# Kernel tuning notes

Measured on AMD Instinct MI355X. Metric: run time of the kernel, lower is better.

Reference implementation:

```python
import jax, jax.numpy as jnp
import numpy as np

B, S, E, H = 4, 2048, 1024, 16
DH = E // H  # 64
DF = 4 * E   # 4096
EPS = 1e-5


def layer_norm(x, g, b):
    mu = jnp.mean(x, axis=-1, keepdims=True)
    var = jnp.mean(jnp.square(x - mu), axis=-1, keepdims=True)
    return (x - mu) * jax.lax.rsqrt(var + EPS) * g + b


def setup_inputs() -> dict:
    key = jax.random.key(0)
    ks = jax.random.split(key, 16)
    s_e = 1.0 / np.sqrt(E)
    s_f = 1.0 / np.sqrt(DF)
    inp = {
        "x": jax.random.normal(ks[0], (B, S, E), jnp.float32),
        # per-head projections stacked over heads: [H, E, DH]
        "wq": jax.random.normal(ks[1], (H, E, DH), jnp.float32) * s_e,
        "wk": jax.random.normal(ks[2], (H, E, DH), jnp.float32) * s_e,
        "wv": jax.random.normal(ks[3], (H, E, DH), jnp.float32) * s_e,
        # output projection [H*DH, E] with bias
        "wo": jax.random.normal(ks[4], (H * DH, E), jnp.float32) * s_e,
        "bo": jax.random.normal(ks[5], (E,), jnp.float32) * 0.01,
        # SwiGLU FFN
        "w1": jax.random.normal(ks[6], (E, DF), jnp.float32) * s_e,
        "b1": jax.random.normal(ks[7], (DF,), jnp.float32) * 0.01,
        "w2": jax.random.normal(ks[8], (E, DF), jnp.float32) * s_e,
        "b2": jax.random.normal(ks[9], (DF,), jnp.float32) * 0.01,
        "w3": jax.random.normal(ks[10], (DF, E), jnp.float32) * s_f,
        "b3": jax.random.normal(ks[11], (E,), jnp.float32) * 0.01,
        # LayerNorm params
        "g1": jnp.ones((E,), jnp.float32),
        "be1": jnp.zeros((E,), jnp.float32),
        "g2": jnp.ones((E,), jnp.float32),
        "be2": jnp.zeros((E,), jnp.float32),
    }
    return inp


def reference(x, wq, wk, wv, wo, bo, w1, b1, w2, b2, w3, b3, g1, be1, g2, be2):
    # --- LN1 + multi-head causal attention ---
    h = layer_norm(x, g1, be1)                       # [B,S,E]
    q = jnp.einsum('bse,hed->bhsd', h, wq)           # [B,H,S,DH]
    k = jnp.einsum('bse,hed->bhsd', h, wk)
    v = jnp.einsum('bse,hed->bhsd', h, wv)
    scores = jnp.einsum('bhsd,bhtd->bhst', q, k) * (DH ** -0.5)  # [B,H,S,S]
    causal = jnp.tril(jnp.ones((S, S), bool))
    scores = jnp.where(causal, scores, -jnp.inf)
    attn = jax.nn.softmax(scores, axis=-1)
    ctx = jnp.einsum('bhst,bhtd->bhsd', attn, v)     # [B,H,S,DH]
    ctx = ctx.transpose(0, 2, 1, 3).reshape(B, S, H * DH)  # concat heads
    attn_out = ctx @ wo + bo                         # [B,S,E]
    r1 = x + attn_out
    # --- LN2 + SwiGLU FFN ---
    h2 = layer_norm(r1, g2, be2)
    a = h2 @ w1 + b1                                 # [B,S,DF]
    gate = h2 @ w2 + b2
    ff = (a * jax.nn.sigmoid(a) * gate) @ w3 + b3    # [B,S,E]
    return r1 + ff
```

## Files before the change

kernel.cpp:

```cpp
#include <hip/hip_runtime.h>
#include <hip/hip_bf16.h>
#include <cstdint>


typedef __bf16 bf16_t;
typedef __attribute__((ext_vector_type(8))) __bf16 bf16x8;
typedef __attribute__((ext_vector_type(4))) __bf16 bf16x4;
typedef __attribute__((ext_vector_type(4))) float f32x4;

#define LOG2E 1.4426950408889634f

static __device__ __forceinline__ void gll16(const void* g, void* l) {
  __builtin_amdgcn_global_load_lds(
      (const __attribute__((address_space(1))) void*)g,
      (__attribute__((address_space(3))) void*)l, 16, 0, 0);
}

template<int PACK>
__global__ __launch_bounds__(256)
void transpose_cvt(const float* __restrict__ in, bf16_t* __restrict__ out,
                   int R, int C, long in_batch, long out_batch, int off)
{
  __shared__ float tile[64][65];
  const float* inp = in + (long)blockIdx.z * in_batch;
  bf16_t* outp = out + (long)blockIdx.z * out_batch;
  const int c0 = blockIdx.x * 64, r0 = blockIdx.y * 64;
  for (int rr = threadIdx.y; rr < 64; rr += 4)
    tile[rr][threadIdx.x] = inp[(long)(r0 + rr) * C + c0 + threadIdx.x];
  __syncthreads();
  for (int cc = threadIdx.y; cc < 64; cc += 4) {
    const int c = c0 + cc;
    const long orow = PACK ? (long)((c >> 4) * 32 + (c & 15) + off) : (long)c;
    outp[orow * R + r0 + threadIdx.x] = (bf16_t)tile[threadIdx.x][cc];
  }
}

template<int BF16IN>
__global__ __launch_bounds__(256)
void ln_kernel(const void* __restrict__ xin, const float* __restrict__ g,
               const float* __restrict__ be, bf16_t* __restrict__ out)
{
  const long row = blockIdx.x;
  float e0, e1, e2, e3;
  if constexpr (BF16IN) {
    const bf16x4 v = ((const bf16x4*)((const bf16_t*)xin + row * 1024))[threadIdx.x];
    e0 = (float)v[0]; e1 = (float)v[1]; e2 = (float)v[2]; e3 = (float)v[3];
  } else {
    const float4 v = ((const float4*)((const float*)xin + row * 1024))[threadIdx.x];
    e0 = v.x; e1 = v.y; e2 = v.z; e3 = v.w;
  }
  float s  = e0 + e1 + e2 + e3;
  float s2 = e0*e0 + e1*e1 + e2*e2 + e3*e3;
  #pragma unroll
  for (int m = 1; m < 64; m <<= 1) {
    s  += __shfl_xor(s, m, 64);
    s2 += __shfl_xor(s2, m, 64);
  }
  __shared__ float red[8];
  const int w = threadIdx.x >> 6, lane = threadIdx.x & 63;
  if (lane == 0) { red[w] = s; red[4 + w] = s2; }
  __syncthreads();
  s  = red[0] + red[1] + red[2] + red[3];
  s2 = red[4] + red[5] + red[6] + red[7];
  const float mu = s * (1.f / 1024.f);
  const float rs = rsqrtf(s2 * (1.f / 1024.f) - mu * mu + 1e-5f);
  const int c = threadIdx.x * 4;
  bf16x4 o;
  o[0] = (bf16_t)((e0 - mu) * rs * g[c+0] + be[c+0]);
  o[1] = (bf16_t)((e1 - mu) * rs * g[c+1] + be[c+1]);
  o[2] = (bf16_t)((e2 - mu) * rs * g[c+2] + be[c+2]);
  o[3] = (bf16_t)((e3 - mu) * rs * g[c+3] + be[c+3]);
  *(bf16x4*)(out + row * 1024 + c) = o;
}

template<int EPI>
__global__ __launch_bounds__(512, 2)
void gemm256(const bf16_t* __restrict__ A, const bf16_t* __restrict__ Bt,
             const float* __restrict__ bias, const float* __restrict__ bias2,
             bf16_t* __restrict__ outB,
             bf16_t* __restrict__ outQ, bf16_t* __restrict__ outK, bf16_t* __restrict__ outV,
             int N)
{
  __shared__ __align__(16) bf16_t Asl[2][2][128 * 64];
  __shared__ __align__(16) bf16_t Bsl[2][2][128 * 64];
  constexpr int KT = 1024;
  constexpr int NT = KT / 64;
  const int tid = threadIdx.x, lane = tid & 63;
  const int w = tid >> 6, wr = w >> 2, wc = w & 3;
  const long row0 = (long)blockIdx.y * 256;
  const long col0 = (long)blockIdx.x * 256;
  const int l15 = lane & 15, lhi = lane >> 4;
  const int offk0 = ((lhi ^ (l15 & 7)) & 7) * 8;
  const int r1 = tid >> 3;
  const int c1 = (tid & 7) ^ (r1 & 7);
  f32x4 acc[8][4] = {};

  auto stageA = [&](int t, int buf) {
    const long kb = (long)t * 64 + c1 * 8;
    #pragma unroll
    for (int h = 0; h < 2; ++h) {
      gll16(A + (row0 + h * 128 + r1) * (long)KT + kb,      (char*)Asl[buf][h] + tid * 16);
      gll16(A + (row0 + h * 128 + r1 + 64) * (long)KT + kb, (char*)Asl[buf][h] + (tid + 512) * 16);
    }
  };
  auto stageB = [&](int t, int buf) {
    const long kb = (long)t * 64 + c1 * 8;
    #pragma unroll
    for (int h = 0; h < 2; ++h) {
      gll16(Bt + (col0 + h * 128 + r1) * (long)KT + kb,      (char*)Bsl[buf][h] + tid * 16);
      gll16(Bt + (col0 + h * 128 + r1 + 64) * (long)KT + kb, (char*)Bsl[buf][h] + (tid + 512) * 16);
    }
  };

  auto ktile = [&](int t, int rb, int wb) {
    if (t + 1 < NT) { stageA(t + 1, wb); stageB(t + 1, wb); }
    const bf16_t* Ah = Asl[rb][wr];
    const bf16_t* Bb = Bsl[rb][wc >> 1] + (wc & 1) * 64 * 64;
    bf16x8 bfr[4][2];
    const bf16_t* bp = Bb + l15 * 64;
    #pragma unroll
    for (int n = 0; n < 4; ++n) {
      bfr[n][0] = *(const bf16x8*)(bp + n * 16 * 64 + offk0);
      bfr[n][1] = *(const bf16x8*)(bp + n * 16 * 64 + (offk0 ^ 32));
    }
    #pragma unroll
    for (int mh = 0; mh < 2; ++mh) {
      bf16x8 af[4][2];
      const bf16_t* ap = Ah + (mh * 64 + l15) * 64;
      #pragma unroll
      for (int m = 0; m < 4; ++m) {
        af[m][0] = *(const bf16x8*)(ap + m * 16 * 64 + offk0);
        af[m][1] = *(const bf16x8*)(ap + m * 16 * 64 + (offk0 ^ 32));
      }
      __builtin_amdgcn_s_setprio(1);
      #pragma unroll
      for (int m = 0; m < 4; ++m)
        #pragma unroll
        for (int n = 0; n < 4; ++n)
          #pragma unroll
          for (int ks = 0; ks < 2; ++ks)
            acc[mh * 4 + m][n] = __builtin_amdgcn_mfma_f32_16x16x32_bf16(
                af[m][ks], bfr[n][ks], acc[mh * 4 + m][n], 0, 0, 0);
      __builtin_amdgcn_s_setprio(0);
    }
    __syncthreads();
  };

  stageA(0, 0);
  stageB(0, 0);
  __syncthreads();

  for (int tt = 0; tt < NT; tt += 2) {
    ktile(tt, 0, 1);
    ktile(tt + 1, 1, 0);
  }

  if constexpr (EPI == 3) {
    const long L0 = ((col0 + wc * 64) >> 5) * 16;
    #pragma unroll
    for (int M = 0; M < 8; ++M) {
      #pragma unroll
      for (int np = 0; np < 2; ++np) {
        const long lc = L0 + np * 16 + l15;
        #pragma unroll
        for (int r = 0; r < 4; ++r) {
          const long rr = row0 + wr * 128 + M * 16 + lhi * 4 + r;
          const float a  = acc[M][2 * np][r] + bias[lc];
          const float gt = acc[M][2 * np + 1][r] + bias2[lc];
          const float sig = 1.0f / (1.0f + __expf(-a));
          outB[rr * N + lc] = (bf16_t)(a * sig * gt);
        }
      }
    }
  } else {
    #pragma unroll
    for (int M = 0; M < 8; ++M) {
      #pragma unroll
      for (int n = 0; n < 4; ++n) {
        const long cc = col0 + wc * 64 + n * 16 + l15;
        #pragma unroll
        for (int r = 0; r < 4; ++r) {
          const long rr = row0 + wr * 128 + M * 16 + lhi * 4 + r;
          const bf16_t bv = (bf16_t)acc[M][n][r];
          const int which = (int)(cc >> 10);
          const int hh = (int)((cc >> 6) & 15);
          const int d  = (int)(cc & 63);
          const long b = rr >> 11, s2 = rr & 2047;
          const long bh = b * 16 + hh;
          if (which == 0)      outQ[(bh * 2048 + s2) * 64 + d] = bv;
          else if (which == 1) outK[(bh * 2048 + s2) * 64 + d] = bv;
          else                 outV[(bh * 64 + d) * 2048 + s2] = bv;
        }
      }
    }
  }
}

template<int EPI, int KT>
__global__ __launch_bounds__(256)
void gemm16(const bf16_t* __restrict__ A, const bf16_t* __restrict__ Bt,
            const float* __restrict__ bias,
            const float* __restrict__ resF, const bf16_t* __restrict__ resB,
            float* __restrict__ outF, bf16_t* __restrict__ outB, int N)
{
  __shared__ __align__(16) bf16_t As[2][128 * 32];
  __shared__ __align__(16) bf16_t Bs[2][128 * 32];
  const int tid = threadIdx.x, lane = tid & 63, w = tid >> 6;
  const int wr = w >> 1, wc = w & 1;
  const long row0 = (long)blockIdx.y * 128;
  const long col0 = (long)blockIdx.x * 128;
  const int rsub = lane >> 2;
  const int csub = (lane & 3) * 8;
  const int kof = (lane >> 4) * 8;
  f32x4 acc[4][4] = {};

  auto stage = [&](long k0, int buf) {
    #pragma unroll
    for (int i = 0; i < 2; ++i) {
      const int c = i * 4 + w;
      gll16(A  + (row0 + c * 16 + rsub) * (long)KT + k0 + csub, (char*)As[buf] + c * 1024);
      gll16(Bt + (col0 + c * 16 + rsub) * (long)KT + k0 + csub, (char*)Bs[buf] + c * 1024);
    }
  };

  stage(0, 0);
  __syncthreads();
  int cur = 0;
  for (long k0 = 0; k0 < KT; k0 += 32) {
    if (k0 + 32 < KT) stage(k0 + 32, cur ^ 1);
    bf16x8 af[4], bfr[4];
    #pragma unroll
    for (int m = 0; m < 4; ++m)
      af[m] = *(const bf16x8*)(As[cur] + (wr * 64 + m * 16 + (lane & 15)) * 32 + kof);
    #pragma unroll
    for (int n = 0; n < 4; ++n)
      bfr[n] = *(const bf16x8*)(Bs[cur] + (wc * 64 + n * 16 + (lane & 15)) * 32 + kof);
    #pragma unroll
    for (int m = 0; m < 4; ++m)
      #pragma unroll
      for (int n = 0; n < 4; ++n)
        acc[m][n] = __builtin_amdgcn_mfma_f32_16x16x32_bf16(af[m], bfr[n], acc[m][n], 0, 0, 0);
    __syncthreads();
    cur ^= 1;
  }
  #pragma unroll
  for (int m = 0; m < 4; ++m) {
    #pragma unroll
    for (int n = 0; n < 4; ++n) {
      const long cc = col0 + wc * 64 + n * 16 + (lane & 15);
      #pragma unroll
      for (int r = 0; r < 4; ++r) {
        const long rr = row0 + wr * 64 + m * 16 + (lane >> 4) * 4 + r;
        const float v = acc[m][n][r];
        if constexpr (EPI == 1) {
          outB[rr * N + cc] = (bf16_t)(v + bias[cc] + resF[rr * N + cc]);
        } else {
          outF[rr * N + cc] = v + bias[cc] + (float)resB[rr * N + cc];
        }
      }
    }
  }
}

__global__ __launch_bounds__(256, 4)
void attn_kernel(const bf16_t* __restrict__ q, const bf16_t* __restrict__ k,
                 const bf16_t* __restrict__ vT, bf16_t* __restrict__ ctx)
{
  __shared__ __align__(16) bf16_t Kb[2][64 * 64];
  __shared__ __align__(16) bf16_t Vb[2][64 * 64];
  __shared__ __align__(16) bf16_t plds[4][16 * 64];
  const int tid = threadIdx.x, lane = tid & 63, wvi = tid >> 6;
  const int bh = blockIdx.x;
  const bf16_t* qp = q  + (long)bh * 2048 * 64;
  const bf16_t* kp = k  + (long)bh * 2048 * 64;
  const bf16_t* vp = vT + (long)bh * 64 * 2048;
  const int l15 = lane & 15, lhi = lane >> 4;
  const long b = bh >> 4;
  const int hh = bh & 15;
  const int sw = (l15 & 7);
  const int psw = sw << 1;

  const int r0s = tid >> 3, cl0 = (tid & 7) ^ (r0s & 7);
  const int r1s = (tid + 256) >> 3, cl1 = (tid & 7) ^ (r1s & 7);

  #pragma unroll
  for (int seg = 0; seg < 2; ++seg) {
    const int ts = (seg == 0) ? blockIdx.y : 31 - blockIdx.y;
    const int qw0 = ts * 64 + wvi * 16;
    const int q_glob = qw0 + l15;
    bf16x8 qf[2];
    #pragma unroll
    for (int kk = 0; kk < 2; ++kk)
      qf[kk] = *(const bf16x8*)(qp + (long)(qw0 + l15) * 64 + kk * 32 + lhi * 8);
    f32x4 accO[4] = {};
    float mrow = -1e30f, lrow = 0.f;

    gll16(kp + (long)(0 + r0s) * 64 + cl0 * 8, (char*)Kb[0] + tid * 16);
    gll16(vp + (long)r0s * 2048 + 0 + cl0 * 8, (char*)Vb[0] + tid * 16);
    gll16(kp + (long)(0 + r1s) * 64 + cl1 * 8, (char*)Kb[0] + (tid + 256) * 16);
    gll16(vp + (long)r1s * 2048 + 0 + cl1 * 8, (char*)Vb[0] + (tid + 256) * 16);
    __syncthreads();

    int cur = 0;
    const int kbmax = ts * 64;
    for (int kb = 0; kb <= kbmax; kb += 64) {
      if (kb + 64 <= kbmax) {
        const int nb = kb + 64;
        gll16(kp + (long)(nb + r0s) * 64 + cl0 * 8, (char*)Kb[cur ^ 1] + tid * 16);
        gll16(vp + (long)r0s * 2048 + nb + cl0 * 8, (char*)Vb[cur ^ 1] + tid * 16);
        gll16(kp + (long)(nb + r1s) * 64 + cl1 * 8, (char*)Kb[cur ^ 1] + (tid + 256) * 16);
        gll16(vp + (long)r1s * 2048 + nb + cl1 * 8, (char*)Vb[cur ^ 1] + (tid + 256) * 16);
      }
      f32x4 accS[4] = {};
      #pragma unroll
      for (int n = 0; n < 4; ++n) {
        const bf16_t* kr = Kb[cur] + (n * 16 + l15) * 64;
        #pragma unroll
        for (int kk = 0; kk < 2; ++kk) {
          const bf16x8 kf = *(const bf16x8*)(kr + ((kk * 4 + lhi) ^ sw) * 8);
          accS[n] = __builtin_amdgcn_mfma_f32_16x16x32_bf16(kf, qf[kk], accS[n], 0, 0, 0);
        }
      }
      const bool needmask = (kb + 63 > qw0);
      float rmax = -1e30f;
      #pragma unroll
      for (int n = 0; n < 4; ++n)
        #pragma unroll
        for (int r = 0; r < 4; ++r) {
          float sv = accS[n][r] * 0.125f;
          if (needmask && (kb + n * 16 + lhi * 4 + r > q_glob)) sv = -1e30f;
          accS[n][r] = sv;
          rmax = fmaxf(rmax, sv);
        }
      rmax = fmaxf(rmax, __shfl_xor(rmax, 16, 64));
      rmax = fmaxf(rmax, __shfl_xor(rmax, 32, 64));
      const float mn = fmaxf(mrow, rmax);
      const float corr = exp2f((mrow - mn) * LOG2E);
      mrow = mn;
      float rsum = 0.f;
      #pragma unroll
      for (int n = 0; n < 4; ++n)
        #pragma unroll
        for (int r = 0; r < 4; ++r) {
          const float p = exp2f((accS[n][r] - mn) * LOG2E);
          accS[n][r] = p;
          rsum += p;
        }
      rsum += __shfl_xor(rsum, 16, 64);
      rsum += __shfl_xor(rsum, 32, 64);
      lrow = lrow * corr + rsum;
      #pragma unroll
      for (int nd = 0; nd < 4; ++nd)
        #pragma unroll
        for (int r = 0; r < 4; ++r) accO[nd][r] *= corr;
      #pragma unroll
      for (int n = 0; n < 4; ++n) {
        bf16x4 pk;
        #pragma unroll
        for (int r = 0; r < 4; ++r) pk[r] = (bf16_t)accS[n][r];
        *(bf16x4*)(&plds[wvi][l15 * 64 + ((4 * n + lhi) ^ psw) * 4]) = pk;
      }
      #pragma unroll
      for (int kk = 0; kk < 2; ++kk) {
        const bf16x8 pf = *(const bf16x8*)(&plds[wvi][l15 * 64 + ((8 * kk + 2 * lhi) ^ psw) * 4]);
        #pragma unroll
        for (int nd = 0; nd < 4; ++nd) {
          const bf16x8 vf = *(const bf16x8*)(Vb[cur] + (nd * 16 + l15) * 64 + ((kk * 4 + lhi) ^ sw) * 8);
          accO[nd] = __builtin_amdgcn_mfma_f32_16x16x32_bf16(vf, pf, accO[nd], 0, 0, 0);
        }
      }
      __syncthreads();
      cur ^= 1;
    }
    const float inv = 1.f / lrow;
    const long crow = (b * 2048 + qw0 + l15) * 1024 + hh * 64;
    #pragma unroll
    for (int nd = 0; nd < 4; ++nd) {
      bf16x4 ok;
      #pragma unroll
      for (int r = 0; r < 4; ++r) ok[r] = (bf16_t)(accO[nd][r] * inv);
      *(bf16x4*)(ctx + crow + nd * 16 + lhi * 4) = ok;
    }
  }
}

extern "C" void kernel_launch(void* const* d_in, const int* in_sizes, int n_in,
                              void* d_out, int out_size, void* d_ws, size_t ws_size,
                              hipStream_t stream)
{
  const float* x   = (const float*)d_in[0];
  const float* wq  = (const float*)d_in[1];
  const float* wk  = (const float*)d_in[2];
  const float* wv  = (const float*)d_in[3];
  const float* wo  = (const float*)d_in[4];
  const float* bo  = (const float*)d_in[5];
  const float* w1  = (const float*)d_in[6];
  const float* b1  = (const float*)d_in[7];
  const float* w2  = (const float*)d_in[8];
  const float* b2  = (const float*)d_in[9];
  const float* w3  = (const float*)d_in[10];
  const float* b3  = (const float*)d_in[11];
  const float* g1  = (const float*)d_in[12];
  const float* be1 = (const float*)d_in[13];
  const float* g2  = (const float*)d_in[14];
  const float* be2 = (const float*)d_in[15];
  float* out = (float*)d_out;

  char* ws = (char*)d_ws;
  bf16_t* h    = (bf16_t*)(ws);
  bf16_t* qb   = (bf16_t*)(ws + 16777216L);
  bf16_t* kb   = (bf16_t*)(ws + 2 * 16777216L);
  bf16_t* vTb  = (bf16_t*)(ws + 3 * 16777216L);
  bf16_t* r1b  = (bf16_t*)(ws + 4 * 16777216L);
  bf16_t* ffin = (bf16_t*)(ws + 4 * 16777216L + 33554432L);
  char* wbase  = ws + 4 * 16777216L + 33554432L + 67108864L;
  bf16_t* Wqkvt = (bf16_t*)(wbase);
  bf16_t* Wot   = (bf16_t*)(wbase + 6291456L);
  bf16_t* Wp    = (bf16_t*)(wbase + 8388608L);
  bf16_t* W3t   = (bf16_t*)(wbase + 25165824L);

  const dim3 tb(64, 4);
  transpose_cvt<0><<<dim3(1, 16, 16), tb, 0, stream>>>(wq, Wqkvt,            1024, 64, 65536, 65536, 0);
  transpose_cvt<0><<<dim3(1, 16, 16), tb, 0, stream>>>(wk, Wqkvt + 1048576L, 1024, 64, 65536, 65536, 0);
  transpose_cvt<0><<<dim3(1, 16, 16), tb, 0, stream>>>(wv, Wqkvt + 2097152L, 1024, 64, 65536, 65536, 0);
  transpose_cvt<0><<<dim3(16, 16, 1), tb, 0, stream>>>(wo, Wot, 1024, 1024, 0, 0, 0);
  transpose_cvt<1><<<dim3(64, 16, 1), tb, 0, stream>>>(w1, Wp, 1024, 4096, 0, 0, 0);
  transpose_cvt<1><<<dim3(64, 16, 1), tb, 0, stream>>>(w2, Wp, 1024, 4096, 0, 0, 16);
  transpose_cvt<0><<<dim3(16, 64, 1), tb, 0, stream>>>(w3, W3t, 4096, 1024, 0, 0, 0);
  ln_kernel<0><<<8192, 256, 0, stream>>>(x, g1, be1, h);
  gemm256<0><<<dim3(12, 32), 512, 0, stream>>>(h, Wqkvt, nullptr, nullptr,
                                               nullptr, qb, kb, vTb, 3072);
  attn_kernel<<<dim3(64, 16), 256, 0, stream>>>(qb, kb, vTb, h);
  gemm16<1, 1024><<<dim3(8, 64), 256, 0, stream>>>(h, Wot, bo, x, nullptr,
                                                   nullptr, r1b, 1024);
  ln_kernel<1><<<8192, 256, 0, stream>>>(r1b, g2, be2, qb);
  gemm256<3><<<dim3(32, 32), 512, 0, stream>>>(qb, Wp, b1, b2,
                                               ffin, nullptr, nullptr, nullptr, 4096);
  gemm16<2, 4096><<<dim3(8, 64), 256, 0, stream>>>(ffin, W3t, b3, nullptr, r1b,
                                                   out, nullptr, 1024);
}
```

Measured before the change: 532.2 us.

## Process 128 query rows per attention block, reusing K/V fragments across two query tiles

Each attention block now covers 128 query rows (each wave handles two 16-row tiles) instead of 64, so the K and V fragments are loaded from LDS into registers once per key block and used by both query tiles. The grid is halved and the launch bound drops to 2 waves per SIMD to make room for the larger register footprint. This cuts LDS read traffic and global K/V loads per query, at the cost of fewer resident blocks and more causal-mask waste on the diagonal tiles.

```diff
diff --git a/kernel.cpp b/kernel.cpp
--- a/kernel.cpp
+++ b/kernel.cpp
@@ -262,7 +262,7 @@
   }
 }
 
-__global__ __launch_bounds__(256, 4)
+__global__ __launch_bounds__(256, 2)
 void attn_kernel(const bf16_t* __restrict__ q, const bf16_t* __restrict__ k,
                  const bf16_t* __restrict__ vT, bf16_t* __restrict__ ctx)
 {
@@ -285,15 +285,16 @@
 
   #pragma unroll
   for (int seg = 0; seg < 2; ++seg) {
-    const int ts = (seg == 0) ? blockIdx.y : 31 - blockIdx.y;
-    const int qw0 = ts * 64 + wvi * 16;
-    const int q_glob = qw0 + l15;
-    bf16x8 qf[2];
-    #pragma unroll
-    for (int kk = 0; kk < 2; ++kk)
-      qf[kk] = *(const bf16x8*)(qp + (long)(qw0 + l15) * 64 + kk * 32 + lhi * 8);
-    f32x4 accO[4] = {};
-    float mrow = -1e30f, lrow = 0.f;
+    const int ts = (seg == 0) ? blockIdx.y : 15 - blockIdx.y;
+    const int qbase = ts * 128 + wvi * 32;
+    bf16x8 qf[2][2];
+    #pragma unroll
+    for (int qt = 0; qt < 2; ++qt)
+      #pragma unroll
+      for (int kk = 0; kk < 2; ++kk)
+        qf[qt][kk] = *(const bf16x8*)(qp + (long)(qbase + qt * 16 + l15) * 64 + kk * 32 + lhi * 8);
+    f32x4 accO[2][4] = {};
+    float mrow[2] = {-1e30f, -1e30f}, lrow[2] = {0.f, 0.f};
 
     gll16(kp + (long)(0 + r0s) * 64 + cl0 * 8, (char*)Kb[0] + tid * 16);
     gll16(vp + (long)r0s * 2048 + 0 + cl0 * 8, (char*)Vb[0] + tid * 16);
@@ -302,7 +303,7 @@
     __syncthreads();
 
     int cur = 0;
-    const int kbmax = ts * 64;
+    const int kbmax = ts * 128 + 64;
     for (int kb = 0; kb <= kbmax; kb += 64) {
       if (kb + 64 <= kbmax) {
         const int nb = kb + 64;
@@ -311,75 +312,88 @@
         gll16(kp + (long)(nb + r1s) * 64 + cl1 * 8, (char*)Kb[cur ^ 1] + (tid + 256) * 16);
         gll16(vp + (long)r1s * 2048 + nb + cl1 * 8, (char*)Vb[cur ^ 1] + (tid + 256) * 16);
       }
-      f32x4 accS[4] = {};
+      bf16x8 kf[4][2], vf[4][2];
       #pragma unroll
       for (int n = 0; n < 4; ++n) {
         const bf16_t* kr = Kb[cur] + (n * 16 + l15) * 64;
+        const bf16_t* vr = Vb[cur] + (n * 16 + l15) * 64;
         #pragma unroll
         for (int kk = 0; kk < 2; ++kk) {
-          const bf16x8 kf = *(const bf16x8*)(kr + ((kk * 4 + lhi) ^ sw) * 8);
-          accS[n] = __builtin_amdgcn_mfma_f32_16x16x32_bf16(kf, qf[kk], accS[n], 0, 0, 0);
-        }
-      }
-      const bool needmask = (kb + 63 > qw0);
-      float rmax = -1e30f;
-      #pragma unroll
-      for (int n = 0; n < 4; ++n)
-        #pragma unroll
-        for (int r = 0; r < 4; ++r) {
-          float sv = accS[n][r] * 0.125f;
-          if (needmask && (kb + n * 16 + lhi * 4 + r > q_glob)) sv = -1e30f;
-          accS[n][r] = sv;
-          rmax = fmaxf(rmax, sv);
-        }
-      rmax = fmaxf(rmax, __shfl_xor(rmax, 16, 64));
-      rmax = fmaxf(rmax, __shfl_xor(rmax, 32, 64));
-      const float mn = fmaxf(mrow, rmax);
-      const float corr = exp2f((mrow - mn) * LOG2E);
-      mrow = mn;
-      float rsum = 0.f;
-      #pragma unroll
-      for (int n = 0; n < 4; ++n)
-        #pragma unroll
-        for (int r = 0; r < 4; ++r) {
-          const float p = exp2f((accS[n][r] - mn) * LOG2E);
-          accS[n][r] = p;
-          rsum += p;
-        }
-      rsum += __shfl_xor(rsum, 16, 64);
-      rsum += __shfl_xor(rsum, 32, 64);
-      lrow = lrow * corr + rsum;
-      #pragma unroll
-      for (int nd = 0; nd < 4; ++nd)
-        #pragma unroll
-        for (int r = 0; r < 4; ++r) accO[nd][r] *= corr;
-      #pragma unroll
-      for (int n = 0; n < 4; ++n) {
-        bf16x4 pk;
-        #pragma unroll
-        for (int r = 0; r < 4; ++r) pk[r] = (bf16_t)accS[n][r];
-        *(bf16x4*)(&plds[wvi][l15 * 64 + ((4 * n + lhi) ^ psw) * 4]) = pk;
-      }
-      #pragma unroll
-      for (int kk = 0; kk < 2; ++kk) {
-        const bf16x8 pf = *(const bf16x8*)(&plds[wvi][l15 * 64 + ((8 * kk + 2 * lhi) ^ psw) * 4]);
-        #pragma unroll
-        for (int nd = 0; nd < 4; ++nd) {
-          const bf16x8 vf = *(const bf16x8*)(Vb[cur] + (nd * 16 + l15) * 64 + ((kk * 4 + lhi) ^ sw) * 8);
-          accO[nd] = __builtin_amdgcn_mfma_f32_16x16x32_bf16(vf, pf, accO[nd], 0, 0, 0);
+          kf[n][kk] = *(const bf16x8*)(kr + ((kk * 4 + lhi) ^ sw) * 8);
+          vf[n][kk] = *(const bf16x8*)(vr + ((kk * 4 + lhi) ^ sw) * 8);
+        }
+      }
+      #pragma unroll
+      for (int qt = 0; qt < 2; ++qt) {
+        f32x4 accS[4] = {};
+        #pragma unroll
+        for (int n = 0; n < 4; ++n)
+          #pragma unroll
+          for (int kk = 0; kk < 2; ++kk)
+            accS[n] = __builtin_amdgcn_mfma_f32_16x16x32_bf16(kf[n][kk], qf[qt][kk], accS[n], 0, 0, 0);
+        const int q0 = qbase + qt * 16;
+        const int q_glob = q0 + l15;
+        const bool needmask = (kb + 63 > q0);
+        float rmax = -1e30f;
+        #pragma unroll
+        for (int n = 0; n < 4; ++n)
+          #pragma unroll
+          for (int r = 0; r < 4; ++r) {
+            float sv = accS[n][r] * 0.125f;
+            if (needmask && (kb + n * 16 + lhi * 4 + r > q_glob)) sv = -1e30f;
+            accS[n][r] = sv;
+            rmax = fmaxf(rmax, sv);
+          }
+        rmax = fmaxf(rmax, __shfl_xor(rmax, 16, 64));
+        rmax = fmaxf(rmax, __shfl_xor(rmax, 32, 64));
+        const float mn = fmaxf(mrow[qt], rmax);
+        const float corr = exp2f((mrow[qt] - mn) * LOG2E);
+        mrow[qt] = mn;
+        float rsum = 0.f;
+        #pragma unroll
+        for (int n = 0; n < 4; ++n)
+          #pragma unroll
+          for (int r = 0; r < 4; ++r) {
+            const float p = exp2f((accS[n][r] - mn) * LOG2E);
+            accS[n][r] = p;
+            rsum += p;
+          }
+        rsum += __shfl_xor(rsum, 16, 64);
+        rsum += __shfl_xor(rsum, 32, 64);
+        lrow[qt] = lrow[qt] * corr + rsum;
+        #pragma unroll
+        for (int nd = 0; nd < 4; ++nd)
+          #pragma unroll
+          for (int r = 0; r < 4; ++r) accO[qt][nd][r] *= corr;
+        #pragma unroll
+        for (int n = 0; n < 4; ++n) {
+          bf16x4 pk;
+          #pragma unroll
+          for (int r = 0; r < 4; ++r) pk[r] = (bf16_t)accS[n][r];
+          *(bf16x4*)(&plds[wvi][l15 * 64 + ((4 * n + lhi) ^ psw) * 4]) = pk;
+        }
+        #pragma unroll
+        for (int kk = 0; kk < 2; ++kk) {
+          const bf16x8 pf = *(const bf16x8*)(&plds[wvi][l15 * 64 + ((8 * kk + 2 * lhi) ^ psw) * 4]);
+          #pragma unroll
+          for (int nd = 0; nd < 4; ++nd)
+            accO[qt][nd] = __builtin_amdgcn_mfma_f32_16x16x32_bf16(vf[nd][kk], pf, accO[qt][nd], 0, 0, 0);
         }
       }
       __syncthreads();
       cur ^= 1;
     }
-    const float inv = 1.f / lrow;
-    const long crow = (b * 2048 + qw0 + l15) * 1024 + hh * 64;
-    #pragma unroll
-    for (int nd = 0; nd < 4; ++nd) {
-      bf16x4 ok;
-      #pragma unroll
-      for (int r = 0; r < 4; ++r) ok[r] = (bf16_t)(accO[nd][r] * inv);
-      *(bf16x4*)(ctx + crow + nd * 16 + lhi * 4) = ok;
+    #pragma unroll
+    for (int qt = 0; qt < 2; ++qt) {
+      const float inv = 1.f / lrow[qt];
+      const long crow = (b * 2048 + qbase + qt * 16 + l15) * 1024 + hh * 64;
+      #pragma unroll
+      for (int nd = 0; nd < 4; ++nd) {
+        bf16x4 ok;
+        #pragma unroll
+        for (int r = 0; r < 4; ++r) ok[r] = (bf16_t)(accO[qt][nd][r] * inv);
+        *(bf16x4*)(ctx + crow + nd * 16 + lhi * 4) = ok;
+      }
     }
   }
 }
@@ -430,7 +444,7 @@
   ln_kernel<0><<<8192, 256, 0, stream>>>(x, g1, be1, h);
   gemm256<0><<<dim3(12, 32), 512, 0, stream>>>(h, Wqkvt, nullptr, nullptr,
                                                nullptr, qb, kb, vTb, 3072);
-  attn_kernel<<<dim3(64, 16), 256, 0, stream>>>(qb, kb, vTb, h);
+  attn_kernel<<<dim3(64, 8), 256, 0, stream>>>(qb, kb, vTb, h);
   gemm16<1, 1024><<<dim3(8, 64), 256, 0, stream>>>(h, Wot, bo, x, nullptr,
                                                    nullptr, r1b, 1024);
   ln_kernel<1><<<8192, 256, 0, stream>>>(r1b, g2, be2, qb);
```

Measured after the change: 560.1 us. 1.05x slower.

## Single-buffer GEMM LDS tiles and request four blocks per CU

Applied to the files above, without the earlier changes.

Drops the double-buffered LDS staging in the 256x256 GEMM to a single buffer, halving shared memory per block, and raises the launch-bounds occupancy hint from 2 to 4 blocks. The k-loop now computes, syncs, issues the next tile's global-to-LDS loads, and syncs again, so loads no longer overlap with MFMA work inside a block. The goal is to hide latency through more resident blocks instead. The risk is that the tighter register budget from the 4-block hint causes spills of the 128-float accumulator, and that the serialized load/compute exposes memory latency.

```diff
diff --git a/kernel.cpp b/kernel.cpp
--- a/kernel.cpp
+++ b/kernel.cpp
@@ -74,15 +74,15 @@
 }
 
 template<int EPI>
-__global__ __launch_bounds__(512, 2)
+__global__ __launch_bounds__(512, 4)
 void gemm256(const bf16_t* __restrict__ A, const bf16_t* __restrict__ Bt,
              const float* __restrict__ bias, const float* __restrict__ bias2,
              bf16_t* __restrict__ outB,
              bf16_t* __restrict__ outQ, bf16_t* __restrict__ outK, bf16_t* __restrict__ outV,
              int N)
 {
-  __shared__ __align__(16) bf16_t Asl[2][2][128 * 64];
-  __shared__ __align__(16) bf16_t Bsl[2][2][128 * 64];
+  __shared__ __align__(16) bf16_t Asl[2][128 * 64];
+  __shared__ __align__(16) bf16_t Bsl[2][128 * 64];
   constexpr int KT = 1024;
   constexpr int NT = KT / 64;
   const int tid = threadIdx.x, lane = tid & 63;
@@ -95,27 +95,30 @@
   const int c1 = (tid & 7) ^ (r1 & 7);
   f32x4 acc[8][4] = {};
 
-  auto stageA = [&](int t, int buf) {
+  auto stageA = [&](int t) {
     const long kb = (long)t * 64 + c1 * 8;
     #pragma unroll
     for (int h = 0; h < 2; ++h) {
-      gll16(A + (row0 + h * 128 + r1) * (long)KT + kb,      (char*)Asl[buf][h] + tid * 16);
-      gll16(A + (row0 + h * 128 + r1 + 64) * (long)KT + kb, (char*)Asl[buf][h] + (tid + 512) * 16);
+      gll16(A + (row0 + h * 128 + r1) * (long)KT + kb,      (char*)Asl[h] + tid * 16);
+      gll16(A + (row0 + h * 128 + r1 + 64) * (long)KT + kb, (char*)Asl[h] + (tid + 512) * 16);
     }
   };
-  auto stageB = [&](int t, int buf) {
+  auto stageB = [&](int t) {
     const long kb = (long)t * 64 + c1 * 8;
     #pragma unroll
     for (int h = 0; h < 2; ++h) {
-      gll16(Bt + (col0 + h * 128 + r1) * (long)KT + kb,      (char*)Bsl[buf][h] + tid * 16);
-      gll16(Bt + (col0 + h * 128 + r1 + 64) * (long)KT + kb, (char*)Bsl[buf][h] + (tid + 512) * 16);
+      gll16(Bt + (col0 + h * 128 + r1) * (long)KT + kb,      (char*)Bsl[h] + tid * 16);
+      gll16(Bt + (col0 + h * 128 + r1 + 64) * (long)KT + kb, (char*)Bsl[h] + (tid + 512) * 16);
     }
   };
 
-  auto ktile = [&](int t, int rb, int wb) {
-    if (t + 1 < NT) { stageA(t + 1, wb); stageB(t + 1, wb); }
-    const bf16_t* Ah = Asl[rb][wr];
-    const bf16_t* Bb = Bsl[rb][wc >> 1] + (wc & 1) * 64 * 64;
+  stageA(0);
+  stageB(0);
+  __syncthreads();
+
+  for (int t = 0; t < NT; ++t) {
+    const bf16_t* Ah = Asl[wr];
+    const bf16_t* Bb = Bsl[wc >> 1] + (wc & 1) * 64 * 64;
     bf16x8 bfr[4][2];
     const bf16_t* bp = Bb + l15 * 64;
     #pragma unroll
@@ -144,15 +147,11 @@
       __builtin_amdgcn_s_setprio(0);
     }
     __syncthreads();
-  };
-
-  stageA(0, 0);
-  stageB(0, 0);
-  __syncthreads();
-
-  for (int tt = 0; tt < NT; tt += 2) {
-    ktile(tt, 0, 1);
-    ktile(tt + 1, 1, 0);
+    if (t + 1 < NT) {
+      stageA(t + 1);
+      stageB(t + 1);
+      __syncthreads();
+    }
   }
 
   if constexpr (EPI == 3) {
```

Result: slower. 1.529 ms (+187.3%).
